# Kernel tuning notes

Measured on AMD Instinct MI355X. Metric: run time of the kernel, lower is better.

## Reference

```python
import jax, jax.numpy as jnp
import numpy as np

B, T, D, H, W = 128, 1024, 32, 64, 128
C = D + 1            # control_size = data_size + 1
O = H * C            # cvf MLP output size


def _linear_params(k, out_f, in_f):
    lim = 1.0 / np.sqrt(in_f)
    kw, kb = jax.random.split(k)
    Wm = jax.random.uniform(kw, (out_f, in_f), minval=-lim, maxval=lim, dtype=jnp.float32)
    b = jax.random.uniform(kb, (out_f,), minval=-lim, maxval=lim, dtype=jnp.float32)
    return Wm, b


def setup_inputs() -> dict:
    key = jax.random.key(0)
    ks = jax.random.split(key, 8)
    # initial MLP: (D+1) -> W -> W -> H, relu hidden
    iW0, ib0 = _linear_params(ks[0], W, D + 1)
    iW1, ib1 = _linear_params(ks[1], W, W)
    iW2, ib2 = _linear_params(ks[2], H, W)
    # cvf MLP: (H+1) -> W -> W -> H*C, lipswish hidden, tanh final
    vW0, vb0 = _linear_params(ks[3], W, H + 1)
    vW1, vb1 = _linear_params(ks[4], W, W)
    vW2, vb2 = _linear_params(ks[5], O, W)
    # readout: H -> 1
    rW, rb = _linear_params(ks[6], 1, H)
    ts = jnp.arange(T, dtype=jnp.float32)
    ys = jax.random.normal(ks[7], (B, T, D), dtype=jnp.float32)
    return dict(ts=ts, ys=ys,
                iW0=iW0, ib0=ib0, iW1=iW1, ib1=ib1, iW2=iW2, ib2=ib2,
                vW0=vW0, vb0=vb0, vW1=vb1 * 0 + vW1, vb1=vb1, vW2=vW2, vb2=vb2,
                rW=rW, rb=rb)


def _lipswish(x):
    return 0.909 * jax.nn.silu(x)


def reference(ts, ys, iW0, ib0, iW1, ib1, iW2, ib2,
              vW0, vb0, vW1, vb1, vW2, vb2, rW, rb):
    b, t_len, d = ys.shape
    h = iW2.shape[0]
    c = d + 1

    def initial_mlp(x):  # [B, D+1] -> [B, H]
        z = jax.nn.relu(x @ iW0.T + ib0)
        z = jax.nn.relu(z @ iW1.T + ib1)
        return z @ iW2.T + ib2

    def vf(t, y):  # scalar t, y [B,H] -> [B,H,C]
        inp = jnp.concatenate([jnp.full((y.shape[0], 1), t, y.dtype), y], axis=1)
        z = _lipswish(inp @ vW0.T + vb0)
        z = _lipswish(z @ vW1.T + vb1)
        out = jnp.tanh(z @ vW2.T + vb2)
        return out.reshape(y.shape[0], h, c)

    # control path values x(t_i) = [t_i, y_i]; no NaNs so interpolation fixups are no-ops
    xs = jnp.concatenate([jnp.broadcast_to(ts[None, :, None], (b, t_len, 1)), ys], axis=2)  # [B,T,C]
    y0 = initial_mlp(xs[:, 0])
    vf0 = vf(ts[0], y0)

    # constant step dt=1 aligned with grid -> control increments are consecutive diffs
    dxs = jnp.swapaxes(xs[:, 1:] - xs[:, :-1], 0, 1)  # [T-1,B,C]
    t1s = ts[1:]

    def step(carry, inp):
        y, yhat, v = carry
        t1, dx = inp
        # ReversibleHeun: yhat1 = 2*y - yhat + f(t0,yhat0)·dx ; y1 = y + 0.5*(f0+f1)·dx
        yhat1 = 2.0 * y - yhat + jnp.einsum('bhc,bc->bh', v, dx)
        v1 = vf(t1, yhat1)
        y1 = y + 0.5 * jnp.einsum('bhc,bc->bh', v + v1, dx)
        return (y1, yhat1, v1), None

    (yT, _, _), _ = jax.lax.scan(step, (y0, y0, vf0), (t1s, dxs))
    return yT @ rW.T + rb  # [B,1]
```

## Files before the change

kernel.cpp:

```cpp
#include <hip/hip_runtime.h>
#include <math.h>

constexpr int kB  = 128;
constexpr int kT  = 1024;
constexpr int kD  = 32;
constexpr int kH  = 64;
constexpr int kW  = 128;
constexpr int kC  = kD + 1;
constexpr int kO  = kH * kC;
constexpr int kIN = kH + 1;
constexpr int BLOCK = 1024;

constexpr int WS_W2  = 0;
constexpr int WS_W1  = 135168;
constexpr int WS_W0  = 143360;
constexpr int WS_SC2 = 147584;
constexpr int WS_SC1 = 149696;
constexpr int WS_SC0 = 149824;
constexpr int WS_TOT = 149952;

__device__ __forceinline__ float fast_sigmoid(float x) { return 1.0f / (1.0f + __expf(-x)); }
__device__ __forceinline__ float lipswish_f(float x)   { return 0.909f * x * fast_sigmoid(x); }
__device__ __forceinline__ float fast_tanh(float x) {
    float ax = fabsf(x);
    float e  = __expf(2.0f * ax);
    float r  = 1.0f - 2.0f / (e + 1.0f);
    return copysignf(r, x);
}
__device__ __forceinline__ float dot4(float4 a, float4 b) {
    return a.x * b.x + a.y * b.y + a.z * b.z + a.w * b.w;
}
__device__ __forceinline__ float fma2i(unsigned u, float z0, float z1, float acc) {
    int lo = (int)(short)(u & 0xffffu);
    int hi = ((int)u) >> 16;
    acc += (float)lo * z0 + (float)hi * z1;
    return acc;
}
__device__ __forceinline__ float fma8i(uint4 u, float4 zl, float4 zh, float acc) {
    acc = fma2i(u.x, zl.x, zl.y, acc);
    acc = fma2i(u.y, zl.z, zl.w, acc);
    acc = fma2i(u.z, zh.x, zh.y, acc);
    acc = fma2i(u.w, zh.z, zh.w, acc);
    return acc;
}
__device__ __forceinline__ int q15(float w, float inv) {
    float q = rintf(w * inv);
    q = fmaxf(-32767.0f, fminf(32767.0f, q));
    return (int)q;
}
__device__ __forceinline__ unsigned pack16(int a, int b) {
    return ((unsigned)a & 0xffffu) | ((unsigned)b << 16);
}

__global__ __launch_bounds__(64)
void prep_kernel(const float* __restrict__ vW0, const float* __restrict__ vW1,
                 const float* __restrict__ vW2, unsigned* __restrict__ ws)
{
    const int row  = blockIdx.x;
    const int lane = threadIdx.x;
    float* scf = (float*)ws;

    if (row < kO) {
        const float* src = vW2 + (size_t)row * kW;
        float m = fmaxf(fabsf(src[lane]), fabsf(src[lane + 64]));
        #pragma unroll
        for (int s = 1; s < 64; s <<= 1) m = fmaxf(m, __shfl_xor(m, s));
        float inv = (m > 0.0f) ? 32767.0f / m : 0.0f;
        if (lane == 0) scf[WS_SC2 + row] = (m > 0.0f) ? m / 32767.0f : 0.0f;
        int w = lane;
        unsigned pk = pack16(q15(src[2 * w], inv), q15(src[2 * w + 1], inv));
        int R = row >> 6, r = row & 63, q = w >> 2, e = w & 3;
        ws[WS_W2 + (((R * 16 + q) * 64 + r) << 2) + e] = pk;
    } else if (row < kO + kW) {
        int r = row - kO;
        const float* src = vW1 + (size_t)r * kW;
        float m = fmaxf(fabsf(src[lane]), fabsf(src[lane + 64]));
        #pragma unroll
        for (int s = 1; s < 64; s <<= 1) m = fmaxf(m, __shfl_xor(m, s));
        float inv = (m > 0.0f) ? 32767.0f / m : 0.0f;
        if (lane == 0) scf[WS_SC1 + r] = (m > 0.0f) ? m / 32767.0f : 0.0f;
        int w = lane;
        ws[WS_W1 + r * 64 + w] = pack16(q15(src[2 * w], inv), q15(src[2 * w + 1], inv));
    } else {
        int r = row - kO - kW;
        const float* src = vW0 + (size_t)r * kIN;
        float m = fabsf(src[lane]);
        if (lane == 0) m = fmaxf(m, fabsf(src[64]));
        #pragma unroll
        for (int s = 1; s < 64; s <<= 1) m = fmaxf(m, __shfl_xor(m, s));
        float inv = (m > 0.0f) ? 32767.0f / m : 0.0f;
        if (lane == 0) scf[WS_SC0 + r] = (m > 0.0f) ? m / 32767.0f : 0.0f;
        if (lane < 33) {
            int c0 = 2 * lane, c1 = 2 * lane + 1;
            int qa = q15(src[c0], inv);
            int qb = (c1 < kIN) ? q15(src[c1], inv) : 0;
            ws[WS_W0 + r * 33 + lane] = pack16(qa, qb);
        }
    }
}

template <int QI>
__global__ __launch_bounds__(BLOCK)
void cde_kernel(
    const float* __restrict__ ts,  const float* __restrict__ ys,
    const float* __restrict__ iW0, const float* __restrict__ ib0,
    const float* __restrict__ iW1, const float* __restrict__ ib1,
    const float* __restrict__ iW2, const float* __restrict__ ib2,
    const float* __restrict__ vW0, const float* __restrict__ vb0,
    const float* __restrict__ vW1, const float* __restrict__ vb1,
    const float* __restrict__ vW2, const float* __restrict__ vb2,
    const float* __restrict__ rW,  const float* __restrict__ rb,
    const unsigned* __restrict__ wsb,
    float* __restrict__ out)
{
    const int b  = blockIdx.x;
    const int t  = threadIdx.x;
    const int r8 = t >> 3;
    const int g  = t & 7;
    const int wv = t >> 6;
    const int ln = t & 63;

    __shared__ __align__(16) float s_v[kO];
    __shared__ __align__(16) float s_z1[kW], s_z2[kW];
    __shared__ __align__(16) float s_inp[kIN + 1];
    __shared__ float s_y[kH], s_yhat[kH], s_e[kH];
    __shared__ float s_dx[kC];

    const float*    ysb   = ys + (size_t)b * kT * kD;
    const uint4*    wsW2q = (const uint4*)(wsb + WS_W2);
    const unsigned* wsW1  = wsb + WS_W1;
    const unsigned* wsW0  = wsb + WS_W0;
    const float*    scf   = (const float*)wsb;

    const float bA  = vb2[t];
    const float bB  = vb2[t + 1024];
    const float bTl = (t < 512) ? vb2[2048 + r8] : 0.0f;
    const float b0r = vb0[r8];
    const float b1r = vb1[r8];
    const float sA  = QI ? scf[WS_SC2 + t] : 0.0f;
    const float sB  = QI ? scf[WS_SC2 + t + 1024] : 0.0f;
    const float sTl = (QI && t < 512) ? scf[WS_SC2 + 2048 + r8] : 0.0f;
    const float s0r = QI ? scf[WS_SC0 + r8] : 0.0f;
    const float s1r = QI ? scf[WS_SC1 + r8] : 0.0f;

    float x_reg = 0.0f, x_next = 0.0f;
    if (t < kC) {
        x_reg  = (t == 0) ? ts[0] : ysb[t - 1];
        x_next = (t == 0) ? ts[1] : ysb[kD + (t - 1)];
        s_dx[t] = x_reg;
    }
    if (t == 0) s_inp[kIN] = 0.0f;
    __syncthreads();

    if (t < kW) {
        const float* wrow = iW0 + t * kC;
        float acc = ib0[t];
        #pragma unroll
        for (int c = 0; c < kC; c++) acc += wrow[c] * s_dx[c];
        s_z1[t] = fmaxf(acc, 0.0f);
    }
    __syncthreads();
    if (t < kW) {
        const float4* wr = (const float4*)(iW1 + t * kW);
        const float4* z4 = (const float4*)s_z1;
        float acc = ib1[t];
        #pragma unroll 8
        for (int q = 0; q < kW / 4; q++) acc += dot4(wr[q], z4[q]);
        s_z2[t] = fmaxf(acc, 0.0f);
    }
    __syncthreads();
    if (t < kH) {
        const float4* wr = (const float4*)(iW2 + t * kW);
        const float4* z4 = (const float4*)s_z2;
        float acc = ib2[t];
        #pragma unroll 8
        for (int q = 0; q < kW / 4; q++) acc += dot4(wr[q], z4[q]);
        s_y[t] = acc; s_yhat[t] = acc;
        s_inp[1 + t] = acc;
    }
    if (t == 0) s_inp[0] = x_reg;
    __syncthreads();

    for (int i = 0; i < kT; i++) {
        {
            float acc = 0.0f;
            if (QI) {
                const unsigned* rowp = wsW0 + r8 * 33;
                #pragma unroll
                for (int m = 0; m < 5; m++) {
                    int p = g + 8 * m;
                    if (p < 33) acc = fma2i(rowp[p], s_inp[2 * p], s_inp[2 * p + 1], acc);
                }
            } else {
                const float* rowp = vW0 + r8 * kIN;
                #pragma unroll
                for (int m = 0; m < 5; m++) {
                    int p = g + 8 * m;
                    if (p < 33) {
                        float w0 = rowp[2 * p];
                        float w1 = (2 * p + 1 < kIN) ? rowp[2 * p + 1] : 0.0f;
                        acc += w0 * s_inp[2 * p] + w1 * s_inp[2 * p + 1];
                    }
                }
            }
            acc += __shfl_xor(acc, 1);
            acc += __shfl_xor(acc, 2);
            acc += __shfl_xor(acc, 4);
            if (g == 0) s_z1[r8] = lipswish_f(b0r + (QI ? s0r * acc : acc));
        }
        __syncthreads();
        {
            float acc = 0.0f;
            #pragma unroll
            for (int m = 0; m < 2; m++) {
                int ch = g + 8 * m;
                int c0 = 8 * ch;
                const float4* z4 = (const float4*)(s_z1 + c0);
                float4 za = z4[0], zb = z4[1];
                if (QI) {
                    uint4 u = *(const uint4*)(wsW1 + r8 * 64 + 4 * ch);
                    acc = fma8i(u, za, zb, acc);
                } else {
                    const float* wr = vW1 + r8 * kW + c0;
                    acc += dot4(*(const float4*)wr, za) + dot4(*(const float4*)(wr + 4), zb);
                }
            }
            acc += __shfl_xor(acc, 1);
            acc += __shfl_xor(acc, 2);
            acc += __shfl_xor(acc, 4);
            if (g == 0) s_z2[r8] = lipswish_f(b1r + (QI ? s1r * acc : acc));
        }
        __syncthreads();
        {
            float acc0 = 0.0f, acc1 = 0.0f;
            if (QI) {
                const uint4* pA = wsW2q + (size_t)(wv * 16) * 64 + ln;
                const uint4* pB = wsW2q + (size_t)((wv + 16) * 16) * 64 + ln;
                #pragma unroll 2
                for (int m = 0; m < 8; m++) {
                    const float4* z4 = (const float4*)(s_z2 + 16 * m);
                    float4 z0 = z4[0], z1 = z4[1], z2 = z4[2], z3 = z4[3];
                    uint4 a0 = pA[(2 * m) * 64],     a1 = pA[(2 * m + 1) * 64];
                    uint4 c0 = pB[(2 * m) * 64],     c1 = pB[(2 * m + 1) * 64];
                    acc0 = fma8i(a0, z0, z1, acc0);
                    acc0 = fma8i(a1, z2, z3, acc0);
                    acc1 = fma8i(c0, z0, z1, acc1);
                    acc1 = fma8i(c1, z2, z3, acc1);
                }
                s_v[t]        = fast_tanh(bA + sA * acc0);
                s_v[t + 1024] = fast_tanh(bB + sB * acc1);
            } else {
                #pragma unroll 2
                for (int m = 0; m < 8; m++) {
                    const float4* z4 = (const float4*)(s_z2 + 16 * m);
                    float4 z0 = z4[0], z1 = z4[1], z2 = z4[2], z3 = z4[3];
                    const float4* rA = (const float4*)(vW2 + (size_t)t * kW + 16 * m);
                    const float4* rB = (const float4*)(vW2 + (size_t)(t + 1024) * kW + 16 * m);
                    acc0 += dot4(rA[0], z0) + dot4(rA[1], z1) + dot4(rA[2], z2) + dot4(rA[3], z3);
                    acc1 += dot4(rB[0], z0) + dot4(rB[1], z1) + dot4(rB[2], z2) + dot4(rB[3], z3);
                }
                s_v[t]        = fast_tanh(bA + acc0);
                s_v[t + 1024] = fast_tanh(bB + acc1);
            }
        }
        if (t < 512) {
            int c0 = 16 * g;
            const float4* z4 = (const float4*)(s_z2 + c0);
            float4 z0 = z4[0], z1 = z4[1], z2 = z4[2], z3 = z4[3];
            float acc = 0.0f;
            if (QI) {
                uint4 u0 = wsW2q[(size_t)(32 * 16 + 2 * g) * 64 + r8];
                uint4 u1 = wsW2q[(size_t)(32 * 16 + 2 * g + 1) * 64 + r8];
                acc = fma8i(u0, z0, z1, acc);
                acc = fma8i(u1, z2, z3, acc);
            } else {
                const float4* wr = (const float4*)(vW2 + (size_t)(2048 + r8) * kW + c0);
                acc += dot4(wr[0], z0) + dot4(wr[1], z1) + dot4(wr[2], z2) + dot4(wr[3], z3);
            }
            acc += __shfl_xor(acc, 1);
            acc += __shfl_xor(acc, 2);
            acc += __shfl_xor(acc, 4);
            if (g == 0) s_v[2048 + r8] = fast_tanh(bTl + (QI ? sTl * acc : acc));
        }
        __syncthreads();

        if (i > 0 && t < kH) {
            const float* vr = s_v + t * kC;
            float acc = 0.0f;
            #pragma unroll
            for (int c = 0; c < kC; c++) acc += vr[c] * s_dx[c];
            s_y[t] += 0.5f * (s_e[t] + acc);
        }
        __syncthreads();

        if (i < kT - 1) {
            if (t < kC) {
                float xi = x_next;
                s_dx[t] = xi - x_reg;
                x_reg = xi;
                if (i + 2 < kT)
                    x_next = (t == 0) ? ts[i + 2] : ysb[(size_t)(i + 2) * kD + (t - 1)];
            }
            __syncthreads();
            if (t < kH) {
                const float* vr = s_v + t * kC;
                float e = 0.0f;
                #pragma unroll
                for (int c = 0; c < kC; c++) e += vr[c] * s_dx[c];
                s_e[t] = e;
                float yh = 2.0f * s_y[t] - s_yhat[t] + e;
                s_yhat[t] = yh;
                s_inp[1 + t] = yh;
            }
            if (t == 0) s_inp[0] = x_reg;
            __syncthreads();
        }
    }

    __syncthreads();
    if (t == 0) {
        float acc = rb[0];
        #pragma unroll
        for (int h = 0; h < kH; h++) acc += s_y[h] * rW[h];
        out[b] = acc;
    }
}

extern "C" void kernel_launch(void* const* d_in, const int* in_sizes, int n_in,
                              void* d_out, int out_size, void* d_ws, size_t ws_size,
                              hipStream_t stream)
{
    const float* ts  = (const float*)d_in[0];
    const float* ys  = (const float*)d_in[1];
    const float* iW0 = (const float*)d_in[2];
    const float* ib0 = (const float*)d_in[3];
    const float* iW1 = (const float*)d_in[4];
    const float* ib1 = (const float*)d_in[5];
    const float* iW2 = (const float*)d_in[6];
    const float* ib2 = (const float*)d_in[7];
    const float* vW0 = (const float*)d_in[8];
    const float* vb0 = (const float*)d_in[9];
    const float* vW1 = (const float*)d_in[10];
    const float* vb1 = (const float*)d_in[11];
    const float* vW2 = (const float*)d_in[12];
    const float* vb2 = (const float*)d_in[13];
    const float* rW  = (const float*)d_in[14];
    const float* rb  = (const float*)d_in[15];
    float* out = (float*)d_out;
    unsigned* ws = (unsigned*)d_ws;

    if (ws_size >= (size_t)WS_TOT * 4) {
        hipLaunchKernelGGL(prep_kernel, dim3(kO + kW + kW), dim3(64), 0, stream,
                           vW0, vW1, vW2, ws);
        hipLaunchKernelGGL((cde_kernel<1>), dim3(kB), dim3(BLOCK), 0, stream,
                           ts, ys, iW0, ib0, iW1, ib1, iW2, ib2,
                           vW0, vb0, vW1, vb1, vW2, vb2, rW, rb, ws, out);
    } else {
        hipLaunchKernelGGL((cde_kernel<0>), dim3(kB), dim3(BLOCK), 0, stream,
                           ts, ys, iW0, ib0, iW1, ib1, iW2, ib2,
                           vW0, vb0, vW1, vb1, vW2, vb2, rW, rb, ws, out);
    }
}
```

Baseline: 6.450 ms.

## Split each batch pair's vector field across four cooperating blocks with global exchange

Adds a sliced kernel where 256 blocks each own a quarter of the output rows of the large vW2 layer, kept resident in LDS as quantized weights, and process two batch items at once. Blocks exchange their yhat slices every time step through tagged 64-bit atomic slots in global memory, spinning with a bounded budget. If the spin budget runs out a flag is set and the original per-batch kernel reruns as a fallback. The aim is to replace per-step global/L2 reads of vW2 with LDS reads and raise the number of active CUs. The cost is a cross-block handoff on every step, and correctness depends on all 256 blocks being co-resident.

After: 9.458 ms. 46.6% more time.

```diff
diff --git a/kernel.cpp b/kernel.cpp
--- a/kernel.cpp
+++ b/kernel.cpp
@@ -9,15 +9,18 @@
 constexpr int kC  = kD + 1;
 constexpr int kO  = kH * kC;
 constexpr int kIN = kH + 1;
-constexpr int BLOCK = 1024;
-
-constexpr int WS_W2  = 0;
-constexpr int WS_W1  = 135168;
-constexpr int WS_W0  = 143360;
-constexpr int WS_SC2 = 147584;
-constexpr int WS_SC1 = 149696;
-constexpr int WS_SC0 = 149824;
-constexpr int WS_TOT = 149952;
+constexpr int RPS = 528;
+
+constexpr int WS_W2    = 0;
+constexpr int WS_W1    = 135168;
+constexpr int WS_W0    = 143360;
+constexpr int WS_SC2   = 147584;
+constexpr int WS_SC1   = 149696;
+constexpr int WS_SC0   = 149824;
+constexpr int WS_R4TOT = 149952;
+constexpr int WS_FLAG  = 149952;
+constexpr int WS_XCH   = 149954;
+constexpr int WS_TOT   = 182724;
 
 __device__ __forceinline__ float fast_sigmoid(float x) { return 1.0f / (1.0f + __expf(-x)); }
 __device__ __forceinline__ float lipswish_f(float x)   { return 0.909f * x * fast_sigmoid(x); }
@@ -54,11 +57,13 @@
 
 __global__ __launch_bounds__(64)
 void prep_kernel(const float* __restrict__ vW0, const float* __restrict__ vW1,
-                 const float* __restrict__ vW2, unsigned* __restrict__ ws)
+                 const float* __restrict__ vW2, unsigned* __restrict__ ws, int zflag)
 {
     const int row  = blockIdx.x;
     const int lane = threadIdx.x;
     float* scf = (float*)ws;
+
+    if (zflag && row == 0 && lane == 0) ws[WS_FLAG] = 0;
 
     if (row < kO) {
         const float* src = vW2 + (size_t)row * kW;
@@ -79,8 +84,8 @@
         for (int s = 1; s < 64; s <<= 1) m = fmaxf(m, __shfl_xor(m, s));
         float inv = (m > 0.0f) ? 32767.0f / m : 0.0f;
         if (lane == 0) scf[WS_SC1 + r] = (m > 0.0f) ? m / 32767.0f : 0.0f;
-        int w = lane;
-        ws[WS_W1 + r * 64 + w] = pack16(q15(src[2 * w], inv), q15(src[2 * w + 1], inv));
+        ws[WS_W1 + r * 64 + lane] =
+            pack16(q15(src[2 * lane], inv), q15(src[2 * lane + 1], inv));
     } else {
         int r = row - kO - kW;
         const float* src = vW0 + (size_t)r * kIN;
@@ -99,8 +104,251 @@
     }
 }
 
-template <int QI>
-__global__ __launch_bounds__(BLOCK)
+__device__ __forceinline__ void xput(unsigned long long* slot, unsigned tag, float v) {
+    unsigned long long pk = ((unsigned long long)tag << 32) |
+                            (unsigned long long)__float_as_uint(v);
+    __hip_atomic_store(slot, pk, __ATOMIC_RELAXED, __HIP_MEMORY_SCOPE_AGENT);
+}
+__device__ __forceinline__ float xget(unsigned long long* slot, unsigned tag,
+                                      int& budget, int& flagged, unsigned* flag) {
+    unsigned long long v = __hip_atomic_load(slot, __ATOMIC_RELAXED,
+                                             __HIP_MEMORY_SCOPE_AGENT);
+    while ((unsigned)(v >> 32) != tag && budget > 0) {
+        --budget;
+        __builtin_amdgcn_s_sleep(1);
+        v = __hip_atomic_load(slot, __ATOMIC_RELAXED, __HIP_MEMORY_SCOPE_AGENT);
+    }
+    if ((unsigned)(v >> 32) != tag && !flagged) {
+        flagged = 1;
+        atomicOr(flag, 1u);
+    }
+    return __uint_as_float((unsigned)v);
+}
+
+__global__ __launch_bounds__(1024)
+void cde_sliced(
+    const float* __restrict__ ts,  const float* __restrict__ ys,
+    const float* __restrict__ iW0, const float* __restrict__ ib0,
+    const float* __restrict__ iW1, const float* __restrict__ ib1,
+    const float* __restrict__ iW2, const float* __restrict__ ib2,
+    const float* __restrict__ vb0, const float* __restrict__ vb1,
+    const float* __restrict__ vb2,
+    const float* __restrict__ rW,  const float* __restrict__ rb,
+    unsigned* __restrict__ wsb, float* __restrict__ out)
+{
+    const int blk = blockIdx.x;
+    const int t   = threadIdx.x;
+    const int g   = blk & 63;
+    const int s   = blk >> 6;
+
+    extern __shared__ unsigned s_w2[];
+    __shared__ __align__(16) float s_z1[2][kW], s_z2[2][kW];
+    __shared__ __align__(16) float s_inp[2][68];
+    __shared__ float s_v[2][RPS];
+    __shared__ float s_y[2][16], s_yh[2][16], s_e[2][16];
+    __shared__ float s_dx[2][2][34];
+    __shared__ float s_yt[2][kH];
+
+    const float*        scf   = (const float*)wsb;
+    const unsigned*     wsW1  = wsb + WS_W1;
+    const unsigned*     wsW0  = wsb + WS_W0;
+    unsigned long long* xch   = (unsigned long long*)(wsb + WS_XCH);
+    unsigned*           flagp = wsb + WS_FLAG;
+
+    const int jj_ = t >> 9;
+    const int r_  = (t >> 2) & 127;
+    const int k4_ = t & 3;
+    const float b0r = vb0[r_], s0r = scf[WS_SC0 + r_];
+    const float b1r = vb1[r_], s1r = scf[WS_SC1 + r_];
+    const float b2a  = (t < 264) ? vb2[s * RPS + t] : 0.0f;
+    const float sc2a = (t < 264) ? scf[WS_SC2 + s * RPS + t] : 0.0f;
+    const float b2b  = (t < 264) ? vb2[s * RPS + t + 264] : 0.0f;
+    const float sc2b = (t < 264) ? scf[WS_SC2 + s * RPS + t + 264] : 0.0f;
+
+    int budget = 1 << 16, flagged = 0;
+
+    for (int idx = t; idx < RPS * 64; idx += 1024) {
+        int row = idx >> 6, w = idx & 63;
+        int grow = s * RPS + row;
+        int q = w >> 2, e = w & 3;
+        s_w2[((q * RPS + row) << 2) + e] =
+            wsb[WS_W2 + ((((grow >> 6) * 16 + q) * 64 + (grow & 63)) << 2) + e];
+    }
+
+    const int jx = t >> 6, cx = t & 63;
+    const float* ysbx = ys + (size_t)(2 * g + (jx & 1)) * kT * kD;
+    float x_reg = 0.0f, x_next = 0.0f;
+    if (t < 128 && cx < kC) {
+        x_reg  = (cx == 0) ? ts[0] : ysbx[cx - 1];
+        x_next = (cx == 0) ? ts[1] : ysbx[kD + (cx - 1)];
+        s_dx[0][jx][cx] = x_reg;
+    }
+    if (t < 2) { s_inp[t][65] = 0.0f; s_inp[t][66] = 0.0f; s_inp[t][67] = 0.0f; }
+    __syncthreads();
+
+    {
+        float acc = 0.0f;
+        #pragma unroll
+        for (int m = 0; m < 9; m++) {
+            int c = k4_ + 4 * m;
+            if (c < kC) acc += iW0[r_ * kC + c] * s_dx[0][jj_][c];
+        }
+        acc += __shfl_xor(acc, 1); acc += __shfl_xor(acc, 2);
+        if (k4_ == 0) s_z1[jj_][r_] = fmaxf(ib0[r_] + acc, 0.0f);
+    }
+    __syncthreads();
+    {
+        float acc = 0.0f;
+        #pragma unroll
+        for (int m = 0; m < 32; m++) {
+            int c = k4_ + 4 * m;
+            acc += iW1[r_ * kW + c] * s_z1[jj_][c];
+        }
+        acc += __shfl_xor(acc, 1); acc += __shfl_xor(acc, 2);
+        if (k4_ == 0) s_z2[jj_][r_] = fmaxf(ib1[r_] + acc, 0.0f);
+    }
+    __syncthreads();
+    {
+        int h = (t >> 3) & 63, k8 = t & 7;
+        float acc = 0.0f;
+        #pragma unroll
+        for (int m = 0; m < 16; m++) {
+            int c = k8 + 8 * m;
+            acc += iW2[h * kW + c] * s_z2[jj_][c];
+        }
+        acc += __shfl_xor(acc, 1); acc += __shfl_xor(acc, 2); acc += __shfl_xor(acc, 4);
+        if (k8 == 0) s_yt[jj_][h] = ib2[h] + acc;
+    }
+    __syncthreads();
+    if (t < 32) {
+        int j = t >> 4, hl = t & 15;
+        float y0 = s_yt[j][16 * s + hl];
+        s_y[j][hl] = y0; s_yh[j][hl] = y0;
+    }
+    if (t < 128) s_inp[t >> 6][1 + (t & 63)] = s_yt[t >> 6][t & 63];
+    if (t < 2)   s_inp[t][0] = ts[0];
+    __syncthreads();
+
+    for (int i = 0; i < kT; i++) {
+        const int cur = i & 1;
+        const int nxt = (i + 1) & 1;
+
+        {
+            float acc = 0.0f;
+            const unsigned* rowp = wsW0 + r_ * 33;
+            #pragma unroll
+            for (int m = 0; m < 9; m++) {
+                int p = k4_ + 4 * m;
+                if (p < 33) {
+                    float2 z = *(const float2*)&s_inp[jj_][2 * p];
+                    acc = fma2i(rowp[p], z.x, z.y, acc);
+                }
+            }
+            acc += __shfl_xor(acc, 1); acc += __shfl_xor(acc, 2);
+            if (k4_ == 0) s_z1[jj_][r_] = lipswish_f(b0r + s0r * acc);
+        }
+        __syncthreads();
+        {
+            float acc = 0.0f;
+            const unsigned* rowp = wsW1 + r_ * 64;
+            #pragma unroll
+            for (int m = 0; m < 16; m++) {
+                int p = k4_ + 4 * m;
+                float2 z = *(const float2*)&s_z1[jj_][2 * p];
+                acc = fma2i(rowp[p], z.x, z.y, acc);
+            }
+            acc += __shfl_xor(acc, 1); acc += __shfl_xor(acc, 2);
+            if (k4_ == 0) s_z2[jj_][r_] = lipswish_f(b1r + s1r * acc);
+        }
+        __syncthreads();
+        if (t < 264) {
+            const uint4* wq4 = (const uint4*)s_w2;
+            float a00 = 0.0f, a01 = 0.0f, a10 = 0.0f, a11 = 0.0f;
+            #pragma unroll 4
+            for (int q = 0; q < 16; q++) {
+                const float4* z0p = (const float4*)&s_z2[0][8 * q];
+                const float4* z1p = (const float4*)&s_z2[1][8 * q];
+                float4 za0 = z0p[0], zb0 = z0p[1];
+                float4 za1 = z1p[0], zb1 = z1p[1];
+                uint4 w0 = wq4[q * RPS + t];
+                uint4 w1 = wq4[q * RPS + t + 264];
+                a00 = fma8i(w0, za0, zb0, a00);
+                a01 = fma8i(w0, za1, zb1, a01);
+                a10 = fma8i(w1, za0, zb0, a10);
+                a11 = fma8i(w1, za1, zb1, a11);
+            }
+            s_v[0][t]       = fast_tanh(b2a + sc2a * a00);
+            s_v[1][t]       = fast_tanh(b2a + sc2a * a01);
+            s_v[0][t + 264] = fast_tanh(b2b + sc2b * a10);
+            s_v[1][t + 264] = fast_tanh(b2b + sc2b * a11);
+        }
+        __syncthreads();
+
+        if (i > 0 && t < 32) {
+            int j = t >> 4, hl = t & 15;
+            const float* vr = &s_v[j][hl * kC];
+            float acc = 0.0f;
+            #pragma unroll
+            for (int c = 0; c < kC; c++) acc += vr[c] * s_dx[cur][j][c];
+            s_y[j][hl] += 0.5f * (s_e[j][hl] + acc);
+        }
+        if (i < kT - 1 && t < 128 && cx < kC) {
+            float xi = x_next;
+            s_dx[nxt][jx][cx] = xi - x_reg;
+            x_reg = xi;
+            if (i + 2 < kT)
+                x_next = (cx == 0) ? ts[i + 2] : ysbx[(size_t)(i + 2) * kD + (cx - 1)];
+        }
+        __syncthreads();
+
+        if (i < kT - 1) {
+            unsigned tag = (unsigned)(i + 1);
+            if (t < 32) {
+                int j = t >> 4, hl = t & 15;
+                const float* vr = &s_v[j][hl * kC];
+                float e = 0.0f;
+                #pragma unroll
+                for (int c = 0; c < kC; c++) e += vr[c] * s_dx[nxt][j][c];
+                s_e[j][hl] = e;
+                float yh = 2.0f * s_y[j][hl] - s_yh[j][hl] + e;
+                s_yh[j][hl] = yh;
+                xput(xch + (((g * 4 + s) * 2 + nxt) << 5) + t, tag, yh);
+            }
+            if (t < 128) {
+                int s2 = t >> 5, w = t & 31;
+                float v = xget(xch + (((g * 4 + s2) * 2 + nxt) << 5) + w,
+                               tag, budget, flagged, flagp);
+                s_inp[w >> 4][1 + s2 * 16 + (w & 15)] = v;
+            }
+            if (t == 128) s_inp[0][0] = ts[i + 1];
+            if (t == 129) s_inp[1][0] = ts[i + 1];
+            __syncthreads();
+        }
+    }
+
+    if (t < 32) {
+        int j = t >> 4, hl = t & 15;
+        xput(xch + (((g * 4 + s) * 2 + 0) << 5) + t, (unsigned)kT, s_y[j][hl]);
+    }
+    if (s == 0) {
+        if (t < 128) {
+            int s2 = t >> 5, w = t & 31;
+            float v = xget(xch + (((g * 4 + s2) * 2 + 0) << 5) + w,
+                           (unsigned)kT, budget, flagged, flagp);
+            s_yt[w >> 4][s2 * 16 + (w & 15)] = v;
+        }
+        __syncthreads();
+        if (t < 2) {
+            float acc = rb[0];
+            #pragma unroll
+            for (int h = 0; h < kH; h++) acc += s_yt[t][h] * rW[h];
+            out[2 * g + t] = acc;
+        }
+    }
+}
+
+template <int QI, int RESCUE>
+__global__ __launch_bounds__(1024)
 void cde_kernel(
     const float* __restrict__ ts,  const float* __restrict__ ys,
     const float* __restrict__ iW0, const float* __restrict__ ib0,
@@ -113,6 +361,8 @@
     const unsigned* __restrict__ wsb,
     float* __restrict__ out)
 {
+    if (RESCUE && wsb[WS_FLAG] == 0u) return;
+
     const int b  = blockIdx.x;
     const int t  = threadIdx.x;
     const int r8 = t >> 3;
@@ -240,8 +490,8 @@
                 for (int m = 0; m < 8; m++) {
                     const float4* z4 = (const float4*)(s_z2 + 16 * m);
                     float4 z0 = z4[0], z1 = z4[1], z2 = z4[2], z3 = z4[3];
-                    uint4 a0 = pA[(2 * m) * 64],     a1 = pA[(2 * m + 1) * 64];
-                    uint4 c0 = pB[(2 * m) * 64],     c1 = pB[(2 * m + 1) * 64];
+                    uint4 a0 = pA[(2 * m) * 64], a1 = pA[(2 * m + 1) * 64];
+                    uint4 c0 = pB[(2 * m) * 64], c1 = pB[(2 * m + 1) * 64];
                     acc0 = fma8i(a0, z0, z1, acc0);
                     acc0 = fma8i(a1, z2, z3, acc0);
                     acc1 = fma8i(c0, z0, z1, acc1);
@@ -264,8 +514,8 @@
             }
         }
         if (t < 512) {
-            int c0 = 16 * g;
-            const float4* z4 = (const float4*)(s_z2 + c0);
+            int c0i = 16 * g;
+            const float4* z4 = (const float4*)(s_z2 + c0i);
             float4 z0 = z4[0], z1 = z4[1], z2 = z4[2], z3 = z4[3];
             float acc = 0.0f;
             if (QI) {
@@ -274,7 +524,7 @@
                 acc = fma8i(u0, z0, z1, acc);
                 acc = fma8i(u1, z2, z3, acc);
             } else {
-                const float4* wr = (const float4*)(vW2 + (size_t)(2048 + r8) * kW + c0);
+                const float4* wr = (const float4*)(vW2 + (size_t)(2048 + r8) * kW + c0i);
                 acc += dot4(wr[0], z0) + dot4(wr[1], z1) + dot4(wr[2], z2) + dot4(wr[3], z3);
             }
             acc += __shfl_xor(acc, 1);
@@ -349,14 +599,28 @@
     float* out = (float*)d_out;
     unsigned* ws = (unsigned*)d_ws;
 
+    constexpr unsigned kDynLds = 16 * RPS * 16;
+
     if (ws_size >= (size_t)WS_TOT * 4) {
         hipLaunchKernelGGL(prep_kernel, dim3(kO + kW + kW), dim3(64), 0, stream,
-                           vW0, vW1, vW2, ws);
-        hipLaunchKernelGGL((cde_kernel<1>), dim3(kB), dim3(BLOCK), 0, stream,
+                           vW0, vW1, vW2, ws, 1);
+        (void)hipFuncSetAttribute(reinterpret_cast<const void*>(cde_sliced),
+                                  hipFuncAttributeMaxDynamicSharedMemorySize,
+                                  (int)kDynLds);
+        hipLaunchKernelGGL(cde_sliced, dim3(256), dim3(1024), kDynLds, stream,
+                           ts, ys, iW0, ib0, iW1, ib1, iW2, ib2,
+                           vb0, vb1, vb2, rW, rb, ws, out);
+        hipLaunchKernelGGL((cde_kernel<1, 1>), dim3(kB), dim3(1024), 0, stream,
+                           ts, ys, iW0, ib0, iW1, ib1, iW2, ib2,
+                           vW0, vb0, vW1, vb1, vW2, vb2, rW, rb, ws, out);
+    } else if (ws_size >= (size_t)WS_R4TOT * 4) {
+        hipLaunchKernelGGL(prep_kernel, dim3(kO + kW + kW), dim3(64), 0, stream,
+                           vW0, vW1, vW2, ws, 0);
+        hipLaunchKernelGGL((cde_kernel<1, 0>), dim3(kB), dim3(1024), 0, stream,
                            ts, ys, iW0, ib0, iW1, ib1, iW2, ib2,
                            vW0, vb0, vW1, vb1, vW2, vb2, rW, rb, ws, out);
     } else {
-        hipLaunchKernelGGL((cde_kernel<0>), dim3(kB), dim3(BLOCK), 0, stream,
+        hipLaunchKernelGGL((cde_kernel<0, 0>), dim3(kB), dim3(1024), 0, stream,
                            ts, ys, iW0, ib0, iW1, ib1, iW2, ib2,
                            vW0, vb0, vW1, vb1, vW2, vb2, rW, rb, ws, out);
     }
```
